# Performance work log

Hardware: AMD Instinct MI355X
Metric: run time of the kernel (lower is better)

The kernel has to match this reference:

```python
import jax, jax.numpy as jnp
import numpy as np

B, N, H = 2, 4096, 1024
HEADS, DHEAD, M = 16, 64, 256
KERNEL_EPS = 1e-3


def setup_inputs() -> dict:
    key = jax.random.key(0)
    ks = jax.random.split(key, 10)
    w = lambda k, shp: jax.random.normal(k, shp, dtype=jnp.float32) * 0.02
    return {
        "hidden_states": jax.random.normal(ks[0], (B, N, H), dtype=jnp.float32),
        "Wq": w(ks[1], (H, H)), "bq": jnp.zeros((H,), jnp.float32),
        "Wk": w(ks[2], (H, H)), "bk": jnp.zeros((H,), jnp.float32),
        "Wv": w(ks[3], (H, H)), "bv": jnp.zeros((H,), jnp.float32),
        "Wo": w(ks[4], (H, H)), "bo": jnp.zeros((H,), jnp.float32),
        "proj": jax.random.normal(ks[5], (M, DHEAD), dtype=jnp.float32),
    }


def _split_heads(x):
    b, n, _ = x.shape
    return x.reshape(b, n, HEADS, DHEAD).transpose(0, 2, 1, 3)  # [b,h,n,d]


def _softmax_kernel(data, proj, is_query):
    # data: [b,h,n,d]; proj: [m,d]
    data_normalizer = DHEAD ** (-0.25)
    data_dash = jnp.einsum('bhnd,md->bhnm', data_normalizer * data, proj)
    diag_data = -0.5 * jnp.sum(data * data, axis=-1, keepdims=True)  # [b,h,n,1]
    if is_query:
        # argmax over a size-1 last dim -> stabilizer == diag_data itself
        stab = diag_data
    else:
        stab = jnp.max(diag_data)
    kernel_out = jnp.exp(diag_data + (data_dash - stab))  # exp kernel: exp(h + x)
    return (M ** (-0.5)) * (kernel_out + KERNEL_EPS)


def _performer_forward(hidden_states, Wq, bq, Wk, bk, Wv, bv, Wo, bo, proj):
    q = _split_heads(jnp.einsum('bni,oi->bno', hidden_states, Wq) + bq)
    k = _split_heads(jnp.einsum('bni,oi->bno', hidden_states, Wk) + bk)
    v = _split_heads(jnp.einsum('bni,oi->bno', hidden_states, Wv) + bv)

    qf = _softmax_kernel(q, proj, is_query=True)   # [b,h,n,m]
    kf = _softmax_kernel(k, proj, is_query=False)  # [b,h,n,m]

    # linear_attention (non-causal FAVOR+)
    k_cumsum = kf.sum(axis=-2)                                   # [b,h,m]
    d_inv = 1.0 / jnp.einsum('bhnm,bhm->bhn', qf, k_cumsum)      # [b,h,n]
    context = jnp.einsum('bhnm,bhne->bhme', kf, v)               # [b,h,m,d]
    out = jnp.einsum('bhme,bhnm,bhn->bhne', context, qf, d_inv)  # [b,h,n,d]

    out = out.transpose(0, 2, 1, 3).reshape(hidden_states.shape[0], -1, H)
    return jnp.einsum('bni,oi->bno', out, Wo) + bo


def reference(hidden_states, Wq, bq, Wk, bk, Wv, bv, Wo, bo, proj):
    return _performer_forward(hidden_states, Wq, bq, Wk, bk, Wv, bv, Wo, bo, proj)
```

## Files before the change

### kernel.cpp

```cpp
#include <hip/hip_runtime.h>
#include <math.h>

#define B_      2
#define N_      4096
#define H_      1024
#define HEADS_  16
#define DH_     64
#define M_      256
#define NSPLIT  8
#define EPAD    80

constexpr float NORMALIZER = 0.35355339059327373f;
constexpr float RATIO      = 0.0625f;
constexpr float KEPS       = 1e-3f;

typedef __bf16 bf16x8 __attribute__((ext_vector_type(8)));
typedef __bf16 bf16x4 __attribute__((ext_vector_type(4)));
typedef float  f32x4  __attribute__((ext_vector_type(4)));

__global__ __launch_bounds__(256) void split_bf16(
    const float* __restrict__ src, __bf16* __restrict__ hi, __bf16* __restrict__ lo)
{
    int i = blockIdx.x * 256 + threadIdx.x;
    float4 v = ((const float4*)src)[i];
    float vv[4] = {v.x, v.y, v.z, v.w};
    bf16x4 h, l;
#pragma unroll
    for (int j = 0; j < 4; ++j) {
        __bf16 hh = (__bf16)vv[j];
        h[j] = hh;
        l[j] = (__bf16)(vv[j] - (float)hh);
    }
    ((bf16x4*)hi)[i] = h;
    ((bf16x4*)lo)[i] = l;
}

__global__ __launch_bounds__(256) void split_w(
    const float* __restrict__ W0, const float* __restrict__ W1,
    const float* __restrict__ W2, const float* __restrict__ W3,
    __bf16* __restrict__ hi, __bf16* __restrict__ lo)
{
    const float* src = W0;
    if (blockIdx.y == 1) src = W1;
    else if (blockIdx.y == 2) src = W2;
    else if (blockIdx.y == 3) src = W3;
    int i = blockIdx.x * 256 + threadIdx.x;
    size_t o = (size_t)blockIdx.y * 262144 + i;
    float4 v = ((const float4*)src)[i];
    float vv[4] = {v.x, v.y, v.z, v.w};
    bf16x4 h, l;
#pragma unroll
    for (int j = 0; j < 4; ++j) {
        __bf16 hh = (__bf16)vv[j];
        h[j] = hh;
        l[j] = (__bf16)(vv[j] - (float)hh);
    }
    ((bf16x4*)hi)[o] = h;
    ((bf16x4*)lo)[o] = l;
}

template<bool BF16OUT>
__global__ __launch_bounds__(512, 4) void gemm_mfma3(
    const __bf16* __restrict__ Ah, const __bf16* __restrict__ Al,
    const __bf16* __restrict__ Bh0, const __bf16* __restrict__ Bl0,
    const __bf16* __restrict__ Bh1, const __bf16* __restrict__ Bl1,
    const __bf16* __restrict__ Bh2, const __bf16* __restrict__ Bl2,
    const float* __restrict__ bi0, const float* __restrict__ bi1, const float* __restrict__ bi2,
    float* __restrict__ C0,
    __bf16* __restrict__ Ch0, __bf16* __restrict__ Cl0,
    __bf16* __restrict__ Ch1, __bf16* __restrict__ Cl1,
    __bf16* __restrict__ Ch2, __bf16* __restrict__ Cl2)
{
    const __bf16* Bh = Bh0; const __bf16* Bl = Bl0; const float* bias = bi0;
    __bf16* Ch = Ch0; __bf16* Cl = Cl0;
    if (blockIdx.z == 1) { Bh = Bh1; Bl = Bl1; bias = bi1; Ch = Ch1; Cl = Cl1; }
    else if (blockIdx.z == 2) { Bh = Bh2; Bl = Bl2; bias = bi2; Ch = Ch2; Cl = Cl2; }

    __shared__ alignas(16) __bf16 lds[2][4][128 * 32];

    const int t    = threadIdx.x;
    const int lane = t & 63;
    const int lm   = lane & 15;
    const int lq   = lane >> 4;
    const int w    = t >> 6;
    const int wm   = (w >> 2) * 64;
    const int wn   = (w & 3) * 32;

    const int wg = blockIdx.x + 8 * blockIdx.y;
    const int sw = (wg & 7) * 64 + (wg >> 3);
    const int n0 = (sw & 7) * 128;
    const int m0 = (sw >> 3) * 128;
    const int K    = 1024;
    const int NK   = 32;

    const int tw = w >> 1;
    const int hw = w & 1;
    const __bf16* mysrc = (tw == 0) ? Ah : (tw == 1) ? Al : (tw == 2) ? Bh : Bl;
    const int     rbase = ((tw < 2) ? m0 : n0) + hw * 64;
    const int rsub   = lane >> 2;
    const int slot   = lane & 3;
    const int schunk = slot ^ ((lane >> 3) & 3);
    const __bf16* gbase = mysrc + (size_t)(rbase + rsub) * K + schunk * 8;

    f32x4 acc[4][2];
#pragma unroll
    for (int i = 0; i < 4; ++i)
#pragma unroll
        for (int j = 0; j < 2; ++j) acc[i][j] = (f32x4){0.f, 0.f, 0.f, 0.f};

    const int swz = (lq ^ ((lm >> 1) & 3)) * 8;

    auto stage = [&](int buf, int k0) {
#pragma unroll
        for (int c = 0; c < 4; ++c) {
            const __bf16* g = gbase + (size_t)c * 16 * K + k0;
            __builtin_amdgcn_global_load_lds(
                (const __attribute__((address_space(1))) void*)g,
                (__attribute__((address_space(3))) void*)&lds[buf][tw][(hw * 64 + c * 16) * 32],
                16, 0, 0);
        }
    };

    auto compute = [&](int p) {
        const __bf16* tAh = lds[p][0];
        const __bf16* tAl = lds[p][1];
        const __bf16* tBh = lds[p][2];
        const __bf16* tBl = lds[p][3];
        bf16x8 bh[2], bl[2];
#pragma unroll
        for (int j = 0; j < 2; ++j) {
            int off = (wn + j * 16 + lm) * 32 + swz;
            bh[j] = *(const bf16x8*)&tBh[off];
            bl[j] = *(const bf16x8*)&tBl[off];
        }
#pragma unroll
        for (int i = 0; i < 4; ++i) {
            int off = (wm + i * 16 + lm) * 32 + swz;
            bf16x8 ah = *(const bf16x8*)&tAh[off];
            bf16x8 al = *(const bf16x8*)&tAl[off];
#pragma unroll
            for (int j = 0; j < 2; ++j) {
                acc[i][j] = __builtin_amdgcn_mfma_f32_16x16x32_bf16(ah, bh[j], acc[i][j], 0, 0, 0);
                acc[i][j] = __builtin_amdgcn_mfma_f32_16x16x32_bf16(al, bh[j], acc[i][j], 0, 0, 0);
                acc[i][j] = __builtin_amdgcn_mfma_f32_16x16x32_bf16(ah, bl[j], acc[i][j], 0, 0, 0);
            }
        }
    };

    stage(0, 0);
    int p = 0;
#pragma unroll 1
    for (int kk = 0; kk < NK - 1; ++kk) {
        stage(p ^ 1, (kk + 1) * 32);
        asm volatile("s_waitcnt vmcnt(4)" ::: "memory");
        asm volatile("s_barrier" ::: "memory");
        compute(p);
        asm volatile("s_barrier" ::: "memory");
        p ^= 1;
    }
    asm volatile("s_waitcnt vmcnt(0)" ::: "memory");
    asm volatile("s_barrier" ::: "memory");
    compute(p);

    float bsr[2];
#pragma unroll
    for (int j = 0; j < 2; ++j) bsr[j] = bias[n0 + wn + j * 16 + lm];
#pragma unroll
    for (int i = 0; i < 4; ++i)
#pragma unroll
        for (int r = 0; r < 4; ++r) {
            int rowm = m0 + wm + i * 16 + lq * 4 + r;
#pragma unroll
            for (int j = 0; j < 2; ++j) {
                int col = n0 + wn + j * 16 + lm;
                float o = acc[i][j][r] + bsr[j];
                if (BF16OUT) {
                    __bf16 hh = (__bf16)o;
                    Ch[(size_t)rowm * 1024 + col] = hh;
                    Cl[(size_t)rowm * 1024 + col] = (__bf16)(o - (float)hh);
                } else {
                    C0[(size_t)rowm * 1024 + col] = o;
                }
            }
        }
}

__global__ __launch_bounds__(256) void diag_kernel(
    const __bf16* __restrict__ Kh, const __bf16* __restrict__ Kl,
    float* __restrict__ diag, float* __restrict__ partials)
{
    int gt = blockIdx.x * 256 + threadIdx.x;
    int r  = gt >> 2;
    int q  = gt & 3;
    const bf16x8* ph = (const bf16x8*)(Kh + (size_t)r * 64 + q * 16);
    const bf16x8* pl = (const bf16x8*)(Kl + (size_t)r * 64 + q * 16);
    float s = 0.f;
#pragma unroll
    for (int i = 0; i < 2; ++i) {
        bf16x8 vh = ph[i], vl = pl[i];
#pragma unroll
        for (int j = 0; j < 8; ++j) {
            float x = (float)vh[j] + (float)vl[j];
            s += x * x;
        }
    }
    s += __shfl_xor(s, 1);
    s += __shfl_xor(s, 2);
    float d = -0.5f * s;
    if (q == 0) {
        int h = r & 15, bn = r >> 4;
        int n = bn & 4095, b = bn >> 12;
        diag[(((size_t)b * 16 + h) << 12) + n] = d;
    }
    __shared__ float red[256];
    red[threadIdx.x] = d;
    __syncthreads();
    for (int s2 = 128; s2 > 0; s2 >>= 1) {
        if (threadIdx.x < s2) red[threadIdx.x] = fmaxf(red[threadIdx.x], red[threadIdx.x + s2]);
        __syncthreads();
    }
    if (threadIdx.x == 0) partials[blockIdx.x] = red[0];
}

__global__ __launch_bounds__(256) void reduce_stab(
    const float* __restrict__ partials, float* __restrict__ stab, int n)
{
    float m = -3.0e38f;
    for (int i = threadIdx.x; i < n; i += 256) m = fmaxf(m, partials[i]);
    __shared__ float red[256];
    red[threadIdx.x] = m;
    __syncthreads();
    for (int s2 = 128; s2 > 0; s2 >>= 1) {
        if (threadIdx.x < s2) red[threadIdx.x] = fmaxf(red[threadIdx.x], red[threadIdx.x + s2]);
        __syncthreads();
    }
    if (threadIdx.x == 0) stab[0] = red[0];
}

__global__ __launch_bounds__(256, 2) void ctx_mfma(
    const __bf16* __restrict__ Kh, const __bf16* __restrict__ Kl,
    const __bf16* __restrict__ Vh, const __bf16* __restrict__ Vl,
    const __bf16* __restrict__ projH, const __bf16* __restrict__ projL,
    const float* __restrict__ diag, const float* __restrict__ stabp,
    float* __restrict__ ctxp)
{
    __shared__ alignas(16) char ldsbuf[59904];
    __shared__ float dg[64];
    __bf16* kfTh = (__bf16*)ldsbuf;
    __bf16* kfTl = kfTh + 9216;
    __bf16* vTh  = kfTl + 9216;
    __bf16* vTl  = vTh + 5760;
    float*  ctxe = (float*)ldsbuf;

    const int t    = threadIdx.x;
    const int lane = t & 63;
    const int w    = t >> 6;
    const int lm   = lane & 15;
    const int lq   = lane >> 4;
    const int bh   = blockIdx.z;
    const int b    = bh >> 4, h = bh & 15;
    const int mh   = blockIdx.y;
    const int slice = blockIdx.x;
    const int mwave = mh * 128 + w * 32;
    const float stab = stabp[0];
    const size_t rowbase = (size_t)b * N_ * H_ + (size_t)h * DH_;
    const float* diag_bh = diag + (size_t)bh * N_;

    for (int idx = t; idx < 16 * 72; idx += 256) {
        int e = 64 + idx / 72, n = idx % 72;
        vTh[e * 72 + n] = (e == 64 && n < 64) ? (__bf16)1.0f : (__bf16)0.0f;
        vTl[e * 72 + n] = (__bf16)0.0f;
    }

    bf16x8 ph[2][2], pl[2][2];
#pragma unroll
    for (int mf = 0; mf < 2; ++mf)
#pragma unroll
        for (int ks = 0; ks < 2; ++ks) {
            size_t pa = (size_t)(mwave + mf * 16 + lm) * 64 + ks * 32 + lq * 8;
            ph[mf][ks] = *(const bf16x8*)(projH + pa);
            pl[mf][ks] = *(const bf16x8*)(projL + pa);
        }

    f32x4 acc[2][5];
#pragma unroll
    for (int mf = 0; mf < 2; ++mf)
#pragma unroll
        for (int ef = 0; ef < 5; ++ef) acc[mf][ef] = (f32x4){0.f, 0.f, 0.f, 0.f};

    const int nl = t >> 2, dc = (t & 3) * 16;
    bf16x8 v0, v1, u0, u1;
    bf16x8 kh_p[4][2], kl_p[4][2];
    {
        const int nbase = slice * (N_ / NSPLIT);
        size_t va = rowbase + (size_t)(nbase + nl) * H_ + dc;
        v0 = *(const bf16x8*)(Vh + va);
        v1 = *(const bf16x8*)(Vh + va + 8);
        u0 = *(const bf16x8*)(Vl + va);
        u1 = *(const bf16x8*)(Vl + va + 8);
#pragma unroll
        for (int nf = 0; nf < 4; ++nf)
#pragma unroll
            for (int ks = 0; ks < 2; ++ks) {
                size_t ka = rowbase + (size_t)(nbase + nf * 16 + lm) * H_ + ks * 32 + lq * 8;
                kh_p[nf][ks] = *(const bf16x8*)(Kh + ka);
                kl_p[nf][ks] = *(const bf16x8*)(Kl + ka);
            }
    }

    for (int tile = 0; tile < 8; ++tile) {
        const int n0 = slice * (N_ / NSPLIT) + tile * 64;
        __syncthreads();

#pragma unroll
        for (int j = 0; j < 8; ++j) {
            vTh[(dc + j) * 72 + nl]     = v0[j];
            vTh[(dc + 8 + j) * 72 + nl] = v1[j];
            vTl[(dc + j) * 72 + nl]     = u0[j];
            vTl[(dc + 8 + j) * 72 + nl] = u1[j];
        }
        if (t < 64) dg[t] = diag_bh[n0 + t] - stab;

        f32x4 dsh[4][2];
#pragma unroll
        for (int nf = 0; nf < 4; ++nf) {
#pragma unroll
            for (int mf = 0; mf < 2; ++mf) dsh[nf][mf] = (f32x4){0.f, 0.f, 0.f, 0.f};
#pragma unroll
            for (int mf = 0; mf < 2; ++mf)
#pragma unroll
                for (int ks = 0; ks < 2; ++ks) {
                    dsh[nf][mf] = __builtin_amdgcn_mfma_f32_16x16x32_bf16(kh_p[nf][ks], ph[mf][ks], dsh[nf][mf], 0, 0, 0);
                    dsh[nf][mf] = __builtin_amdgcn_mfma_f32_16x16x32_bf16(kl_p[nf][ks], ph[mf][ks], dsh[nf][mf], 0, 0, 0);
                    dsh[nf][mf] = __builtin_amdgcn_mfma_f32_16x16x32_bf16(kh_p[nf][ks], pl[mf][ks], dsh[nf][mf], 0, 0, 0);
                }
        }

        __syncthreads();

        if (tile < 7) {
            size_t va = rowbase + (size_t)(n0 + 64 + nl) * H_ + dc;
            v0 = *(const bf16x8*)(Vh + va);
            v1 = *(const bf16x8*)(Vh + va + 8);
            u0 = *(const bf16x8*)(Vl + va);
            u1 = *(const bf16x8*)(Vl + va + 8);
#pragma unroll
            for (int nf = 0; nf < 4; ++nf)
#pragma unroll
                for (int ks = 0; ks < 2; ++ks) {
                    size_t ka = rowbase + (size_t)(n0 + 64 + nf * 16 + lm) * H_ + ks * 32 + lq * 8;
                    kh_p[nf][ks] = *(const bf16x8*)(Kh + ka);
                    kl_p[nf][ks] = *(const bf16x8*)(Kl + ka);
                }
        }

#pragma unroll
        for (int nf = 0; nf < 4; ++nf) {
            float4 dgv = *(const float4*)&dg[nf * 16 + lq * 4];
            float dga[4] = {dgv.x, dgv.y, dgv.z, dgv.w};
#pragma unroll
            for (int mf = 0; mf < 2; ++mf) {
                int mrow = w * 32 + mf * 16 + lm;
                bf16x4 vh_, vl_;
#pragma unroll
                for (int r = 0; r < 4; ++r) {
                    float kf = RATIO * (__expf(dga[r] + NORMALIZER * dsh[nf][mf][r]) + KEPS);
                    __bf16 hh = (__bf16)kf;
                    vh_[r] = hh;
                    vl_[r] = (__bf16)(kf - (float)hh);
                }
                int nbase = nf * 16 + lq * 4;
                *(bf16x4*)&kfTh[mrow * 72 + nbase] = vh_;
                *(bf16x4*)&kfTl[mrow * 72 + nbase] = vl_;
            }
        }

#pragma unroll
        for (int ks = 0; ks < 2; ++ks) {
#pragma unroll
            for (int mf = 0; mf < 2; ++mf) {
                bf16x8 af = *(const bf16x8*)&kfTh[(w * 32 + mf * 16 + lm) * 72 + ks * 32 + lq * 8];
                bf16x8 afl = *(const bf16x8*)&kfTl[(w * 32 + mf * 16 + lm) * 72 + ks * 32 + lq * 8];
#pragma unroll
                for (int ef = 0; ef < 5; ++ef) {
                    bf16x8 bfh = *(const bf16x8*)&vTh[(ef * 16 + lm) * 72 + ks * 32 + lq * 8];
                    bf16x8 bfl = *(const bf16x8*)&vTl[(ef * 16 + lm) * 72 + ks * 32 + lq * 8];
                    acc[mf][ef] = __builtin_amdgcn_mfma_f32_16x16x32_bf16(af,  bfh, acc[mf][ef], 0, 0, 0);
                    acc[mf][ef] = __builtin_amdgcn_mfma_f32_16x16x32_bf16(afl, bfh, acc[mf][ef], 0, 0, 0);
                    acc[mf][ef] = __builtin_amdgcn_mfma_f32_16x16x32_bf16(af,  bfl, acc[mf][ef], 0, 0, 0);
                }
            }
        }
    }

    __syncthreads();
#pragma unroll
    for (int mf = 0; mf < 2; ++mf)
#pragma unroll
        for (int ef = 0; ef < 5; ++ef)
#pragma unroll
            for (int r = 0; r < 4; ++r) {
                int ml = w * 32 + mf * 16 + lq * 4 + r;
                int e  = ef * 16 + lm;
                ctxe[ml * 81 + e] = acc[mf][ef][r];
            }
    __syncthreads();
    const size_t SLICE = (size_t)(B_ * HEADS_) * EPAD * M_;
    const size_t obase = (size_t)slice * SLICE + (size_t)bh * EPAD * M_;
    for (int i = t; i < EPAD * 128; i += 256) {
        int e = i >> 7, ml = i & 127;
        ctxp[obase + (size_t)e * M_ + mh * 128 + ml] = ctxe[ml * 81 + e];
    }
}

__global__ __launch_bounds__(256) void ctx_reduce(
    const float* __restrict__ ctxp, __bf16* __restrict__ ctxTh, __bf16* __restrict__ ctxTl)
{
    int idx = blockIdx.x * 256 + threadIdx.x;
    const size_t SLICE = (size_t)(B_ * HEADS_) * EPAD * M_;
    float s = 0.f;
#pragma unroll
    for (int k = 0; k < NSPLIT; ++k) s += ctxp[(size_t)k * SLICE + idx];
    __bf16 hh = (__bf16)s;
    ctxTh[idx] = hh;
    ctxTl[idx] = (__bf16)(s - (float)hh);
}

__global__ __launch_bounds__(512, 2) void out_mfma(
    const __bf16* __restrict__ Qh, const __bf16* __restrict__ Ql,
    const __bf16* __restrict__ projH, const __bf16* __restrict__ projL,
    const __bf16* __restrict__ ctxTh, const __bf16* __restrict__ ctxTl,
    __bf16* __restrict__ attnH, __bf16* __restrict__ attnL)
{
    __shared__ alignas(16) __bf16 ctxLh[80 * 256];
    __shared__ alignas(16) __bf16 ctxLl[80 * 256];
    __shared__ alignas(16) __bf16 qfh[8][32][72];
    __shared__ alignas(16) __bf16 qfl[8][32][72];

    const int t    = threadIdx.x;
    const int lane = t & 63;
    const int w    = t >> 6;
    const int lm   = lane & 15;
    const int lq   = lane >> 4;
    const int bh   = blockIdx.y;
    const int b    = bh >> 4, h = bh & 15;
    const int nw   = blockIdx.x * 256 + w * 32;
    const size_t rowbase = (size_t)b * N_ * H_ + (size_t)h * DH_;

    const __bf16* cth = ctxTh + (size_t)bh * EPAD * M_;
    const __bf16* ctl = ctxTl + (size_t)bh * EPAD * M_;

    {
        const int r_in = lane >> 5;
        const int cp   = lane & 31;
#pragma unroll
        for (int c = 0; c < 5; ++c) {
            int idx = w * 5 + c;
            int r   = idx * 2 + r_in;
            int gc  = cp ^ (r & 7);
            const __bf16* gh = cth + (size_t)r * 256 + gc * 8;
            const __bf16* gl = ctl + (size_t)r * 256 + gc * 8;
            __builtin_amdgcn_global_load_lds(
                (const __attribute__((address_space(1))) void*)gh,
                (__attribute__((address_space(3))) void*)&ctxLh[idx * 512],
                16, 0, 0);
            __builtin_amdgcn_global_load_lds(
                (const __attribute__((address_space(1))) void*)gl,
                (__attribute__((address_space(3))) void*)&ctxLl[idx * 512],
                16, 0, 0);
        }
    }

    bf16x8 qh_[2][2], ql_[2][2];
#pragma unroll
    for (int nf = 0; nf < 2; ++nf)
#pragma unroll
        for (int ks = 0; ks < 2; ++ks) {
            size_t qa = rowbase + (size_t)(nw + nf * 16 + lm) * H_ + ks * 32 + lq * 8;
            qh_[nf][ks] = *(const bf16x8*)(Qh + qa);
            ql_[nf][ks] = *(const bf16x8*)(Ql + qa);
        }

    __syncthreads();

    f32x4 accO[2][5];
#pragma unroll
    for (int nf = 0; nf < 2; ++nf)
#pragma unroll
        for (int ef = 0; ef < 5; ++ef) accO[nf][ef] = (f32x4){0.f, 0.f, 0.f, 0.f};

#pragma unroll
    for (int mc = 0; mc < 4; ++mc) {
        const int m0 = mc * 64;
        f32x4 dsh[2][4];
#pragma unroll
        for (int nf = 0; nf < 2; ++nf)
#pragma unroll
            for (int mf = 0; mf < 4; ++mf) dsh[nf][mf] = (f32x4){0.f, 0.f, 0.f, 0.f};
#pragma unroll
        for (int mf = 0; mf < 4; ++mf)
#pragma unroll
            for (int ks = 0; ks < 2; ++ks) {
                size_t pa = (size_t)(m0 + mf * 16 + lm) * 64 + ks * 32 + lq * 8;
                bf16x8 ph = *(const bf16x8*)(projH + pa);
                bf16x8 pl = *(const bf16x8*)(projL + pa);
#pragma unroll
                for (int nf = 0; nf < 2; ++nf) {
                    dsh[nf][mf] = __builtin_amdgcn_mfma_f32_16x16x32_bf16(qh_[nf][ks], ph, dsh[nf][mf], 0, 0, 0);
                    dsh[nf][mf] = __builtin_amdgcn_mfma_f32_16x16x32_bf16(ql_[nf][ks], ph, dsh[nf][mf], 0, 0, 0);
                    dsh[nf][mf] = __builtin_amdgcn_mfma_f32_16x16x32_bf16(qh_[nf][ks], pl, dsh[nf][mf], 0, 0, 0);
                }
            }
#pragma unroll
        for (int nf = 0; nf < 2; ++nf)
#pragma unroll
            for (int mf = 0; mf < 4; ++mf)
#pragma unroll
                for (int r = 0; r < 4; ++r) {
                    float qf = RATIO * (__expf(NORMALIZER * dsh[nf][mf][r]) + KEPS);
                    __bf16 hh = (__bf16)qf;
                    int nloc = nf * 16 + lq * 4 + r;
                    qfh[w][nloc][mf * 16 + lm] = hh;
                    qfl[w][nloc][mf * 16 + lm] = (__bf16)(qf - (float)hh);
                }
#pragma unroll
        for (int ks = 0; ks < 2; ++ks) {
            bf16x8 af[2], afl[2];
#pragma unroll
            for (int nf = 0; nf < 2; ++nf) {
                af[nf]  = *(const bf16x8*)&qfh[w][nf * 16 + lm][ks * 32 + lq * 8];
                afl[nf] = *(const bf16x8*)&qfl[w][nf * 16 + lm][ks * 32 + lq * 8];
            }
#pragma unroll
            for (int ef = 0; ef < 5; ++ef) {
                int row = ef * 16 + lm;
                int sc  = ((m0 >> 3) + ks * 4 + lq) ^ (lm & 7);
                int off = row * 256 + sc * 8;
                bf16x8 bfh = *(const bf16x8*)&ctxLh[off];
                bf16x8 bfl = *(const bf16x8*)&ctxLl[off];
#pragma unroll
                for (int nf = 0; nf < 2; ++nf) {
                    accO[nf][ef] = __builtin_amdgcn_mfma_f32_16x16x32_bf16(af[nf],  bfh, accO[nf][ef], 0, 0, 0);
                    accO[nf][ef] = __builtin_amdgcn_mfma_f32_16x16x32_bf16(afl[nf], bfh, accO[nf][ef], 0, 0, 0);
                    accO[nf][ef] = __builtin_amdgcn_mfma_f32_16x16x32_bf16(af[nf],  bfl, accO[nf][ef], 0, 0, 0);
                }
            }
        }
    }

#pragma unroll
    for (int nf = 0; nf < 2; ++nf) {
        float dinv[4];
#pragma unroll
        for (int r = 0; r < 4; ++r) {
            float den = __shfl(accO[nf][4][r], lane & 48);
            dinv[r] = 1.f / den;
        }
#pragma unroll
        for (int ef = 0; ef < 4; ++ef)
#pragma unroll
            for (int r = 0; r < 4; ++r) {
                float o = accO[nf][ef][r] * dinv[r];
                __bf16 hh = (__bf16)o;
                size_t oa = rowbase + (size_t)(nw + nf * 16 + lq * 4 + r) * H_ + ef * 16 + lm;
                attnH[oa] = hh;
                attnL[oa] = (__bf16)(o - (float)hh);
            }
    }
}

extern "C" void kernel_launch(void* const* d_in, const int* in_sizes, int n_in,
                              void* d_out, int out_size, void* d_ws, size_t ws_size,
                              hipStream_t stream) {
    const float* hs   = (const float*)d_in[0];
    const float* Wq   = (const float*)d_in[1];
    const float* bq   = (const float*)d_in[2];
    const float* Wk   = (const float*)d_in[3];
    const float* bk   = (const float*)d_in[4];
    const float* Wv   = (const float*)d_in[5];
    const float* bv   = (const float*)d_in[6];
    const float* Wo   = (const float*)d_in[7];
    const float* bo   = (const float*)d_in[8];
    const float* proj = (const float*)d_in[9];
    float* out = (float*)d_out;

    const size_t QSZ = (size_t)B_ * N_ * H_;
    const size_t WSZ = (size_t)H_ * H_;
    const size_t CTXT = (size_t)B_ * HEADS_ * EPAD * M_;

    __bf16* Qh  = (__bf16*)d_ws;
    __bf16* Ql  = Qh + QSZ;
    __bf16* Kh  = Ql + QSZ;
    __bf16* Kl  = Kh + QSZ;
    __bf16* Vh  = Kl + QSZ;
    __bf16* Vl  = Vh + QSZ;
    __bf16* hsH = Vl + QSZ;
    __bf16* hsL = hsH + QSZ;
    __bf16* WH  = hsL + QSZ;
    __bf16* WL  = WH + 4 * WSZ;
    __bf16* projH = WL + 4 * WSZ;
    __bf16* projL = projH + (size_t)M_ * DH_;
    __bf16* ctxTh = projL + (size_t)M_ * DH_;
    __bf16* ctxTl = ctxTh + CTXT;
    float*  diag  = (float*)(ctxTl + CTXT);
    float*  parts = diag + (size_t)B_ * HEADS_ * N_;
    float*  stab  = parts + 2048;
    float*  ctxp  = stab + 16;

    __bf16 *WqH = WH, *WkH = WH + WSZ, *WvH = WH + 2*WSZ, *WoH = WH + 3*WSZ;
    __bf16 *WqL = WL, *WkL = WL + WSZ, *WvL = WL + 2*WSZ, *WoL = WL + 3*WSZ;

    split_bf16<<<QSZ / 4 / 256, 256, 0, stream>>>(hs, hsH, hsL);
    split_w<<<dim3(WSZ / 4 / 256, 4), 256, 0, stream>>>(Wq, Wk, Wv, Wo, WH, WL);
    split_bf16<<<(M_ * DH_) / 4 / 256, 256, 0, stream>>>(proj, projH, projL);

    gemm_mfma3<true><<<dim3(H_ / 128, (B_ * N_) / 128, 3), 512, 0, stream>>>(
        hsH, hsL, WqH, WqL, WkH, WkL, WvH, WvL, bq, bk, bv,
        nullptr, Qh, Ql, Kh, Kl, Vh, Vl);

    diag_kernel<<<2048, 256, 0, stream>>>(Kh, Kl, diag, parts);
    reduce_stab<<<1, 256, 0, stream>>>(parts, stab, 2048);

    ctx_mfma<<<dim3(NSPLIT, 2, B_ * HEADS_), 256, 0, stream>>>(
        Kh, Kl, Vh, Vl, projH, projL, diag, stab, ctxp);

    ctx_reduce<<<(B_ * HEADS_ * EPAD * M_) / 256, 256, 0, stream>>>(ctxp, ctxTh, ctxTl);

    out_mfma<<<dim3(N_ / 256, B_ * HEADS_), 512, 0, stream>>>(
        Qh, Ql, projH, projL, ctxTh, ctxTl, hsH, hsL);

    gemm_mfma3<false><<<dim3(H_ / 128, (B_ * N_) / 128, 1), 512, 0, stream>>>(
        hsH, hsL, WoH, WoL, WoH, WoL, WoH, WoL, bo, bo, bo,
        out, nullptr, nullptr, nullptr, nullptr, nullptr, nullptr);
}
```

Baseline: 417.9 us.

## Fuse Q/K/V projections into one GEMM sharing the activation tile

```diff
diff --git a/kernel.cpp b/kernel.cpp
--- a/kernel.cpp
+++ b/kernel.cpp
@@ -59,24 +59,15 @@
     ((bf16x4*)lo)[o] = l;
 }
 
-template<bool BF16OUT>
-__global__ __launch_bounds__(512, 4) void gemm_mfma3(
+__global__ __launch_bounds__(512, 2) void gemm_qkv(
     const __bf16* __restrict__ Ah, const __bf16* __restrict__ Al,
-    const __bf16* __restrict__ Bh0, const __bf16* __restrict__ Bl0,
-    const __bf16* __restrict__ Bh1, const __bf16* __restrict__ Bl1,
-    const __bf16* __restrict__ Bh2, const __bf16* __restrict__ Bl2,
-    const float* __restrict__ bi0, const float* __restrict__ bi1, const float* __restrict__ bi2,
-    float* __restrict__ C0,
-    __bf16* __restrict__ Ch0, __bf16* __restrict__ Cl0,
-    __bf16* __restrict__ Ch1, __bf16* __restrict__ Cl1,
-    __bf16* __restrict__ Ch2, __bf16* __restrict__ Cl2)
-{
-    const __bf16* Bh = Bh0; const __bf16* Bl = Bl0; const float* bias = bi0;
-    __bf16* Ch = Ch0; __bf16* Cl = Cl0;
-    if (blockIdx.z == 1) { Bh = Bh1; Bl = Bl1; bias = bi1; Ch = Ch1; Cl = Cl1; }
-    else if (blockIdx.z == 2) { Bh = Bh2; Bl = Bl2; bias = bi2; Ch = Ch2; Cl = Cl2; }
-
-    __shared__ alignas(16) __bf16 lds[2][4][128 * 32];
+    const __bf16* __restrict__ WH, const __bf16* __restrict__ WL,
+    const float* __restrict__ bq, const float* __restrict__ bk, const float* __restrict__ bv,
+    __bf16* __restrict__ Qh, __bf16* __restrict__ Ql,
+    __bf16* __restrict__ Kh, __bf16* __restrict__ Kl,
+    __bf16* __restrict__ Vh, __bf16* __restrict__ Vl)
+{
+    __shared__ alignas(16) __bf16 lds[2][8][128 * 32];
 
     const int t    = threadIdx.x;
     const int lane = t & 63;
@@ -90,8 +81,128 @@
     const int sw = (wg & 7) * 64 + (wg >> 3);
     const int n0 = (sw & 7) * 128;
     const int m0 = (sw >> 3) * 128;
-    const int K    = 1024;
-    const int NK   = 32;
+    const int K  = 1024;
+    const int NK = 32;
+    const size_t WSZ = (size_t)H_ * H_;
+
+    const __bf16* mysrc;
+    if      (w == 0) mysrc = Ah;
+    else if (w == 1) mysrc = Al;
+    else             mysrc = ((w & 1) ? WL : WH) + (size_t)((w - 2) >> 1) * WSZ;
+    const int rbase  = (w < 2) ? m0 : n0;
+    const int rsub   = lane >> 2;
+    const int slot   = lane & 3;
+    const int schunk = slot ^ ((lane >> 3) & 3);
+    const __bf16* gbase = mysrc + (size_t)(rbase + rsub) * K + schunk * 8;
+
+    f32x4 acc[3][4][2];
+#pragma unroll
+    for (int s = 0; s < 3; ++s)
+#pragma unroll
+        for (int i = 0; i < 4; ++i)
+#pragma unroll
+            for (int j = 0; j < 2; ++j) acc[s][i][j] = (f32x4){0.f, 0.f, 0.f, 0.f};
+
+    const int swz = (lq ^ ((lm >> 1) & 3)) * 8;
+
+    auto stage = [&](int buf, int k0) {
+#pragma unroll
+        for (int c = 0; c < 8; ++c) {
+            const __bf16* g = gbase + (size_t)c * 16 * K + k0;
+            __builtin_amdgcn_global_load_lds(
+                (const __attribute__((address_space(1))) void*)g,
+                (__attribute__((address_space(3))) void*)&lds[buf][w][c * 512],
+                16, 0, 0);
+        }
+    };
+
+    auto compute = [&](int p) {
+        bf16x8 bh[3][2], bl[3][2];
+#pragma unroll
+        for (int s = 0; s < 3; ++s)
+#pragma unroll
+            for (int j = 0; j < 2; ++j) {
+                int off = (wn + j * 16 + lm) * 32 + swz;
+                bh[s][j] = *(const bf16x8*)&lds[p][2 + 2 * s][off];
+                bl[s][j] = *(const bf16x8*)&lds[p][3 + 2 * s][off];
+            }
+#pragma unroll
+        for (int i = 0; i < 4; ++i) {
+            int off = (wm + i * 16 + lm) * 32 + swz;
+            bf16x8 ah = *(const bf16x8*)&lds[p][0][off];
+            bf16x8 al = *(const bf16x8*)&lds[p][1][off];
+#pragma unroll
+            for (int s = 0; s < 3; ++s)
+#pragma unroll
+                for (int j = 0; j < 2; ++j) {
+                    acc[s][i][j] = __builtin_amdgcn_mfma_f32_16x16x32_bf16(ah, bh[s][j], acc[s][i][j], 0, 0, 0);
+                    acc[s][i][j] = __builtin_amdgcn_mfma_f32_16x16x32_bf16(al, bh[s][j], acc[s][i][j], 0, 0, 0);
+                    acc[s][i][j] = __builtin_amdgcn_mfma_f32_16x16x32_bf16(ah, bl[s][j], acc[s][i][j], 0, 0, 0);
+                }
+        }
+    };
+
+    stage(0, 0);
+    int p = 0;
+#pragma unroll 1
+    for (int kk = 0; kk < NK - 1; ++kk) {
+        stage(p ^ 1, (kk + 1) * 32);
+        asm volatile("s_waitcnt vmcnt(8)" ::: "memory");
+        asm volatile("s_barrier" ::: "memory");
+        compute(p);
+        asm volatile("s_barrier" ::: "memory");
+        p ^= 1;
+    }
+    asm volatile("s_waitcnt vmcnt(0)" ::: "memory");
+    asm volatile("s_barrier" ::: "memory");
+    compute(p);
+
+    const float* biases[3] = {bq, bk, bv};
+    __bf16* Chs[3] = {Qh, Kh, Vh};
+    __bf16* Cls[3] = {Ql, Kl, Vl};
+#pragma unroll
+    for (int s = 0; s < 3; ++s) {
+        float bsr[2];
+#pragma unroll
+        for (int j = 0; j < 2; ++j) bsr[j] = biases[s][n0 + wn + j * 16 + lm];
+#pragma unroll
+        for (int i = 0; i < 4; ++i)
+#pragma unroll
+            for (int r = 0; r < 4; ++r) {
+                int rowm = m0 + wm + i * 16 + lq * 4 + r;
+#pragma unroll
+                for (int j = 0; j < 2; ++j) {
+                    int col = n0 + wn + j * 16 + lm;
+                    float o = acc[s][i][j][r] + bsr[j];
+                    __bf16 hh = (__bf16)o;
+                    Chs[s][(size_t)rowm * 1024 + col] = hh;
+                    Cls[s][(size_t)rowm * 1024 + col] = (__bf16)(o - (float)hh);
+                }
+            }
+    }
+}
+
+__global__ __launch_bounds__(512, 4) void gemm_out(
+    const __bf16* __restrict__ Ah, const __bf16* __restrict__ Al,
+    const __bf16* __restrict__ Bh, const __bf16* __restrict__ Bl,
+    const float* __restrict__ bias, float* __restrict__ C0)
+{
+    __shared__ alignas(16) __bf16 lds[2][4][128 * 32];
+
+    const int t    = threadIdx.x;
+    const int lane = t & 63;
+    const int lm   = lane & 15;
+    const int lq   = lane >> 4;
+    const int w    = t >> 6;
+    const int wm   = (w >> 2) * 64;
+    const int wn   = (w & 3) * 32;
+
+    const int wg = blockIdx.x + 8 * blockIdx.y;
+    const int sw = (wg & 7) * 64 + (wg >> 3);
+    const int n0 = (sw & 7) * 128;
+    const int m0 = (sw >> 3) * 128;
+    const int K  = 1024;
+    const int NK = 32;
 
     const int tw = w >> 1;
     const int hw = w & 1;
@@ -173,14 +284,7 @@
 #pragma unroll
             for (int j = 0; j < 2; ++j) {
                 int col = n0 + wn + j * 16 + lm;
-                float o = acc[i][j][r] + bsr[j];
-                if (BF16OUT) {
-                    __bf16 hh = (__bf16)o;
-                    Ch[(size_t)rowm * 1024 + col] = hh;
-                    Cl[(size_t)rowm * 1024 + col] = (__bf16)(o - (float)hh);
-                } else {
-                    C0[(size_t)rowm * 1024 + col] = o;
-                }
+                C0[(size_t)rowm * 1024 + col] = acc[i][j][r] + bsr[j];
             }
         }
 }
@@ -607,16 +711,14 @@
     float*  stab  = parts + 2048;
     float*  ctxp  = stab + 16;
 
-    __bf16 *WqH = WH, *WkH = WH + WSZ, *WvH = WH + 2*WSZ, *WoH = WH + 3*WSZ;
-    __bf16 *WqL = WL, *WkL = WL + WSZ, *WvL = WL + 2*WSZ, *WoL = WL + 3*WSZ;
+    __bf16 *WoH = WH + 3*WSZ, *WoL = WL + 3*WSZ;
 
     split_bf16<<<QSZ / 4 / 256, 256, 0, stream>>>(hs, hsH, hsL);
     split_w<<<dim3(WSZ / 4 / 256, 4), 256, 0, stream>>>(Wq, Wk, Wv, Wo, WH, WL);
     split_bf16<<<(M_ * DH_) / 4 / 256, 256, 0, stream>>>(proj, projH, projL);
 
-    gemm_mfma3<true><<<dim3(H_ / 128, (B_ * N_) / 128, 3), 512, 0, stream>>>(
-        hsH, hsL, WqH, WqL, WkH, WkL, WvH, WvL, bq, bk, bv,
-        nullptr, Qh, Ql, Kh, Kl, Vh, Vl);
+    gemm_qkv<<<dim3(H_ / 128, (B_ * N_) / 128), 512, 0, stream>>>(
+        hsH, hsL, WH, WL, bq, bk, bv, Qh, Ql, Kh, Kl, Vh, Vl);
 
     diag_kernel<<<2048, 256, 0, stream>>>(Kh, Kl, diag, parts);
     reduce_stab<<<1, 256, 0, stream>>>(parts, stab, 2048);
@@ -629,7 +731,6 @@
     out_mfma<<<dim3(N_ / 256, B_ * HEADS_), 512, 0, stream>>>(
         Qh, Ql, projH, projL, ctxTh, ctxTl, hsH, hsL);
 
-    gemm_mfma3<false><<<dim3(H_ / 128, (B_ * N_) / 128, 1), 512, 0, stream>>>(
-        hsH, hsL, WoH, WoL, WoH, WoL, WoH, WoL, bo, bo, bo,
-        out, nullptr, nullptr, nullptr, nullptr, nullptr, nullptr);
-}
+    gemm_out<<<dim3(H_ / 128, (B_ * N_) / 128), 512, 0, stream>>>(
+        hsH, hsL, WoH, WoL, bo, out);
+}
```

Measured after the change: 420.0 us. No clear change (+0.5%).
